# Kernel tuning notes

Measured on AMD Instinct MI355X. Metric: run time of the kernel, lower is better.

Reference implementation:

```python
import jax, jax.numpy as jnp
import numpy as np

NUM_EMBEDDINGS = 8192
EMBEDDING_DIM = 256
COMMITMENT_COST = 0.25
DECAY = 0.99
EPS = 1e-05


def setup_inputs() -> dict:
    key = jax.random.key(0)
    k1, k2, k3 = jax.random.split(key, 3)
    x = jax.random.normal(k1, (16, 256, 32, 32), dtype=jnp.float32)
    emb = jax.random.normal(k2, (NUM_EMBEDDINGS, EMBEDDING_DIM), dtype=jnp.float32) * 0.1
    emb = emb / jnp.linalg.norm(emb, axis=1, keepdims=True)  # F.normalize(dim=1)
    return {
        "x": x,
        "embedding": emb,
        "cluster_size": jnp.ones((NUM_EMBEDDINGS,), dtype=jnp.float32),
        "embed_avg": emb,
    }


def reference(x, embedding, cluster_size, embed_avg):
    K, D = embedding.shape
    n = x.ndim
    # permute channels (dim 1) to last, flatten to [N, D]
    perm_fwd = (0,) + tuple(range(2, n)) + (1,)
    px = jnp.transpose(x, perm_fwd)
    flat = px.reshape(-1, D)  # [N, D]

    # squared L2 distances (monotone in cdist p=2) -> argmin nearest code
    d = (
        jnp.sum(flat * flat, axis=1, keepdims=True)
        - 2.0 * (flat @ embedding.T)
        + jnp.sum(embedding * embedding, axis=1)
    )  # [N, K]
    idx = jnp.argmin(d, axis=1)  # [N]

    # gather-by-index instead of one-hot @ embedding (same math)
    quantized = embedding[idx].reshape(px.shape)
    perm_back = (0, n - 1) + tuple(range(1, n - 1))
    quantized = jnp.transpose(quantized, perm_back)  # back to x layout

    # EMA buffer updates (training path, no_grad in torch)
    counts = jax.ops.segment_sum(
        jnp.ones_like(idx, dtype=flat.dtype), idx, num_segments=K
    )  # == encodings.sum(0)
    new_cluster_size = cluster_size * DECAY + (1.0 - DECAY) * counts
    dw = jax.ops.segment_sum(flat, idx, num_segments=K)  # == encodings.T @ flat
    new_embed_avg = embed_avg * DECAY + (1.0 - DECAY) * dw
    new_embedding = new_embed_avg / jnp.maximum(new_cluster_size, EPS)[:, None]

    # commitment loss (quantized detached)
    loss = COMMITMENT_COST * jnp.mean((x - jax.lax.stop_gradient(quantized)) ** 2)

    # straight-through estimator
    quantized_st = x + jax.lax.stop_gradient(quantized - x)

    avg_probs = counts / flat.shape[0]  # == encodings.mean(0)
    perplexity = jnp.exp(-jnp.sum(avg_probs * jnp.log(avg_probs + 1e-10)))

    return (quantized_st, loss, perplexity, new_embedding, new_cluster_size, new_embed_avg)
```

## Files before the change

### kernel.cpp

```cpp
#include <hip/hip_runtime.h>
#include <stdint.h>

#define K_CODES 8192
#define D 256
#define NROWS 16384
#define NELEM 4194304

#define WS_ENORM   0x00000u
#define WS_KEYS    0x08000u
#define WS_ICOUNTS 0x28000u
#define WS_CURSOR  0x30000u
#define WS_BASE    0x38000u
#define WS_ROWLIST 0x40000u
#define WS_PART    0x50000u
#define WS_XHI     0x60000u
#define WS_XLO     (WS_XHI + 0x800000u)
#define WS_EHI     (WS_XLO + 0x800000u)
#define WS_ELO     (WS_EHI + 0x400000u)

#define O_QST  0
#define O_LOSS 4194304
#define O_PERP 4194305
#define O_EMB  4194306
#define O_CS   6291458
#define O_EAVG 6299650

typedef unsigned short u16;
typedef __attribute__((ext_vector_type(8))) short bf16x8;
typedef __attribute__((ext_vector_type(4))) float f32x4;

__device__ __forceinline__ u16 f2bf(float f) {
    uint32_t u = __float_as_uint(f);
    u += 0x7FFFu + ((u >> 16) & 1u);
    return (u16)(u >> 16);
}
__device__ __forceinline__ float bf2f(u16 h) {
    return __uint_as_float(((uint32_t)h) << 16);
}

__device__ __forceinline__ void glds16(const u16* g, u16* lds_base) {
    __builtin_amdgcn_global_load_lds(
        (const __attribute__((address_space(1))) uint32_t*)g,
        (__attribute__((address_space(3))) uint32_t*)lds_base, 16, 0, 0);
}

__global__ __launch_bounds__(256) void prep_emb_kernel(const float* __restrict__ emb,
                                                       u16* __restrict__ eh,
                                                       u16* __restrict__ el,
                                                       float* __restrict__ enorm) {
    const int k = blockIdx.x, t = threadIdx.x;
    const size_t i = (size_t)k * D + t;
    const float v = emb[i];
    const u16 h = f2bf(v);
    const float r = v - bf2f(h);
    eh[i] = h;
    el[i] = f2bf(r);
    float s = v * v;
#pragma unroll
    for (int off = 32; off; off >>= 1) s += __shfl_down(s, off, 64);
    __shared__ float sm[4];
    if ((t & 63) == 0) sm[t >> 6] = s;
    __syncthreads();
    if (t == 0) enorm[k] = sm[0] + sm[1] + sm[2] + sm[3];
}

__global__ __launch_bounds__(256) void prep_x_kernel(const float* __restrict__ x,
                                                     u16* __restrict__ xhi,
                                                     u16* __restrict__ xlo) {
    __shared__ u16 Lh[64][72];
    __shared__ u16 Ll[64][72];
    const int hw0 = blockIdx.x << 6;
    const int c0 = blockIdx.y << 6;
    const int b = blockIdx.z;
    const int t = threadIdx.x, l = t & 63, w = t >> 6;
#pragma unroll
    for (int i = 0; i < 16; ++i) {
        const int cl = w * 16 + i;
        const float v = x[(((size_t)(b * 256 + c0 + cl)) << 10) + hw0 + l];
        const u16 h = f2bf(v);
        Lh[l][cl] = h;
        Ll[l][cl] = f2bf(v - bf2f(h));
    }
    __syncthreads();
    const int r = t >> 2, cs = t & 3;
    const size_t n = (((size_t)b) << 10) + hw0 + r;
    const size_t o = n * D + c0 + cs * 16;
    *(uint4*)&xhi[o]     = *(const uint4*)&Lh[r][cs * 16];
    *(uint4*)&xhi[o + 8] = *(const uint4*)&Lh[r][cs * 16 + 8];
    *(uint4*)&xlo[o]     = *(const uint4*)&Ll[r][cs * 16];
    *(uint4*)&xlo[o + 8] = *(const uint4*)&Ll[r][cs * 16 + 8];
}

#define BM 128
#define BN 128
#define BK 32
#define SLICES 8
#define CT_PER 8

__global__ __launch_bounds__(256) void dist_kernel(const u16* __restrict__ xhi,
                                                   const u16* __restrict__ xlo,
                                                   const u16* __restrict__ ehi,
                                                   const u16* __restrict__ elo,
                                                   const float* __restrict__ enorm,
                                                   unsigned long long* __restrict__ keys) {
    __shared__ __align__(16) u16 Ah[BM * BK];
    __shared__ __align__(16) u16 Al[BM * BK];
    __shared__ __align__(16) u16 Bh[BN * BK];
    __shared__ __align__(16) u16 Bl[BN * BK];

    const int tid = threadIdx.x;
    const int l = tid & 63, w = tid >> 6;
    const int wr = w >> 1, wc = w & 1;
    const int slice = blockIdx.x;
    const int n0 = blockIdx.y * BM;
    const int md = l & 15, quad = l >> 4;

    const int c0s = w * 64 + l;
    const int row0 = c0s >> 2, s0 = c0s & 3;
    const int g0 = (s0 - ((row0 >> 1) & 3)) & 3;
    const int c1s = 256 + w * 64 + l;
    const int row1 = c1s >> 2, s1 = c1s & 3;
    const int g1 = (s1 - ((row1 >> 1) & 3)) & 3;
    const int ldsb0 = w * 512;
    const int ldsb1 = 2048 + w * 512;
    const size_t aoff0 = (size_t)(n0 + row0) * D + g0 * 8;
    const size_t aoff1 = (size_t)(n0 + row1) * D + g1 * 8;

    const int sA = (quad + ((md >> 1) & 3)) & 3;

    float rbv[4][4];
    int rbi[4][4];
#pragma unroll
    for (int i = 0; i < 4; ++i)
#pragma unroll
        for (int r = 0; r < 4; ++r) { rbv[i][r] = 1e30f; rbi[i][r] = 0; }

    for (int ct = 0; ct < CT_PER; ++ct) {
        const int cbase = (slice * CT_PER + ct) * BN;
        const size_t boff0 = (size_t)(cbase + row0) * D + g0 * 8;
        const size_t boff1 = (size_t)(cbase + row1) * D + g1 * 8;

        f32x4 acc[4][4];
#pragma unroll
        for (int i = 0; i < 4; ++i)
#pragma unroll
            for (int j = 0; j < 4; ++j) acc[i][j] = (f32x4)0.f;

        for (int kt = 0; kt < D / BK; ++kt) {
            const int kc = kt * BK;
            __syncthreads();
            glds16(xhi + aoff0 + kc, &Ah[ldsb0]);
            glds16(xhi + aoff1 + kc, &Ah[ldsb1]);
            glds16(xlo + aoff0 + kc, &Al[ldsb0]);
            glds16(xlo + aoff1 + kc, &Al[ldsb1]);
            glds16(ehi + boff0 + kc, &Bh[ldsb0]);
            glds16(ehi + boff1 + kc, &Bh[ldsb1]);
            glds16(elo + boff0 + kc, &Bl[ldsb0]);
            glds16(elo + boff1 + kc, &Bl[ldsb1]);
            __syncthreads();

            bf16x8 ah[4], al4[4], bh4[4], bl4[4];
#pragma unroll
            for (int i = 0; i < 4; ++i) {
                const int ra = (wr * 64 + i * 16 + md) * BK + sA * 8;
                const int rb = (wc * 64 + i * 16 + md) * BK + sA * 8;
                ah[i]  = *(const bf16x8*)&Ah[ra];
                al4[i] = *(const bf16x8*)&Al[ra];
                bh4[i] = *(const bf16x8*)&Bh[rb];
                bl4[i] = *(const bf16x8*)&Bl[rb];
            }
#pragma unroll
            for (int i = 0; i < 4; ++i)
#pragma unroll
                for (int j = 0; j < 4; ++j) {
                    acc[i][j] = __builtin_amdgcn_mfma_f32_16x16x32_bf16(ah[i],  bh4[j], acc[i][j], 0, 0, 0);
                    acc[i][j] = __builtin_amdgcn_mfma_f32_16x16x32_bf16(ah[i],  bl4[j], acc[i][j], 0, 0, 0);
                    acc[i][j] = __builtin_amdgcn_mfma_f32_16x16x32_bf16(al4[i], bh4[j], acc[i][j], 0, 0, 0);
                }
        }

        float ec[4];
#pragma unroll
        for (int j = 0; j < 4; ++j) ec[j] = enorm[cbase + wc * 64 + j * 16 + md];
#pragma unroll
        for (int i = 0; i < 4; ++i)
#pragma unroll
            for (int r = 0; r < 4; ++r)
#pragma unroll
                for (int j = 0; j < 4; ++j) {
                    const float s = fmaf(-2.f, acc[i][j][r], ec[j]);
                    const int ci = cbase + wc * 64 + j * 16 + md;
                    if (s < rbv[i][r]) { rbv[i][r] = s; rbi[i][r] = ci; }
                }
    }

#pragma unroll
    for (int i = 0; i < 4; ++i)
#pragma unroll
        for (int r = 0; r < 4; ++r) {
            float bv = rbv[i][r];
            int bi = rbi[i][r];
#pragma unroll
            for (int m = 1; m < 16; m <<= 1) {
                const float ov = __shfl_xor(bv, m, 64);
                const int oi = __shfl_xor(bi, m, 64);
                if (ov < bv || (ov == bv && oi < bi)) { bv = ov; bi = oi; }
            }
            if (md == 0) {
                unsigned int u = __float_as_uint(bv);
                u = (u & 0x80000000u) ? ~u : (u | 0x80000000u);
                const unsigned long long key = ((unsigned long long)u << 32) | (unsigned int)bi;
                atomicMin(&keys[n0 + wr * 64 + i * 16 + quad * 4 + r], key);
            }
        }
}

__global__ __launch_bounds__(256) void quant_loss_kernel(const float* __restrict__ x,
                                                         const float* __restrict__ emb,
                                                         const unsigned long long* __restrict__ keys,
                                                         float* __restrict__ out,
                                                         float* __restrict__ partials,
                                                         int* __restrict__ icounts) {
    const int blk = blockIdx.x;
    const int b = blk >> 4;
    const int hw0 = (blk & 15) << 6;
    const int l = threadIdx.x & 63;
    const int cq = threadIdx.x >> 6;
    const int hw = hw0 + l;
    const int n = (b << 10) + hw;
    const int code = (int)(keys[n] & 0xFFFFFFFFull);
    if (threadIdx.x < 64) atomicAdd(&icounts[code], 1);
    const float* erow = emb + (size_t)code * D;
    const float* xb = x + (((size_t)b * 256) << 10) + hw;
    float* ob = out + O_QST + (((size_t)b * 256) << 10) + hw;
    float lsum = 0.f;
#pragma unroll 4
    for (int c = cq; c < D; c += 4) {
        const float xv = xb[(size_t)c << 10];
        const float ev = erow[c];
        ob[(size_t)c << 10] = xv + (ev - xv);
        const float d = xv - ev;
        lsum = fmaf(d, d, lsum);
    }
    __shared__ float sm[4];
    const int lane = threadIdx.x & 63, wv = threadIdx.x >> 6;
#pragma unroll
    for (int off = 32; off; off >>= 1) lsum += __shfl_down(lsum, off, 64);
    if (lane == 0) sm[wv] = lsum;
    __syncthreads();
    if (threadIdx.x == 0) partials[blockIdx.x] = sm[0] + sm[1] + sm[2] + sm[3];
}

__global__ __launch_bounds__(256) void scan_final_kernel(const int* __restrict__ icounts,
                                                         int* __restrict__ basearr,
                                                         const float* __restrict__ partials,
                                                         float* __restrict__ out) {
    const int t = threadIdx.x, lane = t & 63, w = t >> 6;
    int loc = 0;
    float ps = 0.f;
    for (int i = 0; i < 32; ++i) {
        const int c = icounts[t * 32 + i];
        loc += c;
        const float p = (float)c * (1.0f / 16384.0f);
        ps += p * logf(p + 1e-10f);
    }
    int v = loc;
#pragma unroll
    for (int off = 1; off < 64; off <<= 1) {
        const int u = __shfl_up(v, off, 64);
        if (lane >= off) v += u;
    }
    __shared__ int wsum[4];
    __shared__ float fs[8];
    if (lane == 63) wsum[w] = v;
    float lp = partials[t];
#pragma unroll
    for (int off = 32; off; off >>= 1) {
        lp += __shfl_down(lp, off, 64);
        ps += __shfl_down(ps, off, 64);
    }
    if (lane == 0) { fs[w] = lp; fs[4 + w] = ps; }
    __syncthreads();
    int pre = 0;
    for (int i = 0; i < w; ++i) pre += wsum[i];
    int b = pre + v - loc;
    for (int i = 0; i < 32; ++i) {
        basearr[t * 32 + i] = b;
        b += icounts[t * 32 + i];
    }
    if (t == 0) {
        out[O_LOSS] = 0.25f * ((fs[0] + fs[1] + fs[2] + fs[3]) / 4194304.0f);
        out[O_PERP] = expf(-(fs[4] + fs[5] + fs[6] + fs[7]));
    }
}

__global__ __launch_bounds__(256) void slot_kernel(const unsigned long long* __restrict__ keys,
                                                   const int* __restrict__ basearr,
                                                   int* __restrict__ cursor,
                                                   int* __restrict__ rowlist) {
    const int n = blockIdx.x * 256 + threadIdx.x;
    const int code = (int)(keys[n] & 0xFFFFFFFFull);
    const int pos = atomicAdd(&cursor[code], 1);
    rowlist[basearr[code] + pos] = n;
}

__global__ __launch_bounds__(256) void gather_ema_kernel(const u16* __restrict__ xhi,
                                                         const u16* __restrict__ xlo,
                                                         const int* __restrict__ icounts,
                                                         const int* __restrict__ basearr,
                                                         const int* __restrict__ rowlist,
                                                         const float* __restrict__ embed_avg,
                                                         const float* __restrict__ cluster_size,
                                                         float* __restrict__ out) {
    const int k = blockIdx.x, c = threadIdx.x;
    const int cnt = icounts[k], b0 = basearr[k];
    float s = 0.f;
    for (int t = 0; t < cnt; ++t) {
        const int n = rowlist[b0 + t];
        s += bf2f(xhi[(size_t)n * D + c]) + bf2f(xlo[(size_t)n * D + c]);
    }
    const float ncs = cluster_size[k] * 0.99f + 0.01f * (float)cnt;
    const size_t i = (size_t)k * D + c;
    const float na = embed_avg[i] * 0.99f + 0.01f * s;
    out[O_EAVG + i] = na;
    out[O_EMB + i] = na / fmaxf(ncs, 1e-5f);
    if (c == 0) out[O_CS + k] = ncs;
}

extern "C" void kernel_launch(void* const* d_in, const int* in_sizes, int n_in,
                              void* d_out, int out_size, void* d_ws, size_t ws_size,
                              hipStream_t stream) {
    const float* x            = (const float*)d_in[0];
    const float* emb          = (const float*)d_in[1];
    const float* cluster_size = (const float*)d_in[2];
    const float* embed_avg    = (const float*)d_in[3];
    float* out = (float*)d_out;
    char* ws = (char*)d_ws;

    float* enorm = (float*)(ws + WS_ENORM);
    unsigned long long* keys = (unsigned long long*)(ws + WS_KEYS);
    int* icounts = (int*)(ws + WS_ICOUNTS);
    int* cursor = (int*)(ws + WS_CURSOR);
    int* basearr = (int*)(ws + WS_BASE);
    int* rowlist = (int*)(ws + WS_ROWLIST);
    float* partials = (float*)(ws + WS_PART);
    u16* xhi = (u16*)(ws + WS_XHI);
    u16* xlo = (u16*)(ws + WS_XLO);
    u16* ehi = (u16*)(ws + WS_EHI);
    u16* elo = (u16*)(ws + WS_ELO);

    hipMemsetAsync(ws + WS_ICOUNTS, 0, 0x10000, stream);
    hipMemsetAsync(ws + WS_KEYS, 0xFF, NROWS * 8, stream);

    prep_emb_kernel<<<K_CODES, 256, 0, stream>>>(emb, ehi, elo, enorm);
    prep_x_kernel<<<dim3(16, 4, 16), 256, 0, stream>>>(x, xhi, xlo);
    dist_kernel<<<dim3(SLICES, NROWS / BM), 256, 0, stream>>>(xhi, xlo, ehi, elo, enorm, keys);
    quant_loss_kernel<<<256, 256, 0, stream>>>(x, emb, keys, out, partials, icounts);
    scan_final_kernel<<<1, 256, 0, stream>>>(icounts, basearr, partials, out);
    slot_kernel<<<NROWS / 256, 256, 0, stream>>>(keys, basearr, cursor, rowlist);
    gather_ema_kernel<<<K_CODES, 256, 0, stream>>>(xhi, xlo, icounts, basearr, rowlist,
                                                   embed_avg, cluster_size, out);
}
```

Before: 358.1 us.

## Keep full X row tile resident in LDS and double-buffer codebook chunks

The distance kernel now loads the whole 128-row hi/lo X tile (all 256 dims) into 160KB of dynamic LDS once per block, instead of reloading it for every codebook tile. Codebook hi/lo chunks are streamed into a double buffer with one barrier per k-step, so the next chunk's load overlaps the current MFMAs. The grid shrinks to 2 slices of 32 code tiles each, with XOR-swizzled LDS layouts. This cuts redundant global and LDS traffic for X, at the cost of one block per CU and fewer blocks in flight.

Result: faster. 298.7 us (-16.6%).

```diff
diff --git a/kernel.cpp b/kernel.cpp
--- a/kernel.cpp
+++ b/kernel.cpp
@@ -93,20 +93,16 @@
 
 #define BM 128
 #define BN 128
-#define BK 32
-#define SLICES 8
-#define CT_PER 8
-
-__global__ __launch_bounds__(256) void dist_kernel(const u16* __restrict__ xhi,
-                                                   const u16* __restrict__ xlo,
-                                                   const u16* __restrict__ ehi,
-                                                   const u16* __restrict__ elo,
-                                                   const float* __restrict__ enorm,
-                                                   unsigned long long* __restrict__ keys) {
-    __shared__ __align__(16) u16 Ah[BM * BK];
-    __shared__ __align__(16) u16 Al[BM * BK];
-    __shared__ __align__(16) u16 Bh[BN * BK];
-    __shared__ __align__(16) u16 Bl[BN * BK];
+#define SLICES 2
+#define CT_PER 32
+
+__global__ __launch_bounds__(256, 1) void dist_kernel(const u16* __restrict__ xhi,
+                                                      const u16* __restrict__ xlo,
+                                                      const u16* __restrict__ ehi,
+                                                      const u16* __restrict__ elo,
+                                                      const float* __restrict__ enorm,
+                                                      unsigned long long* __restrict__ keys) {
+    extern __shared__ __align__(16) u16 lds[];
 
     const int tid = threadIdx.x;
     const int l = tid & 63, w = tid >> 6;
@@ -115,18 +111,42 @@
     const int n0 = blockIdx.y * BM;
     const int md = l & 15, quad = l >> 4;
 
-    const int c0s = w * 64 + l;
-    const int row0 = c0s >> 2, s0 = c0s & 3;
-    const int g0 = (s0 - ((row0 >> 1) & 3)) & 3;
-    const int c1s = 256 + w * 64 + l;
-    const int row1 = c1s >> 2, s1 = c1s & 3;
-    const int g1 = (s1 - ((row1 >> 1) & 3)) & 3;
-    const int ldsb0 = w * 512;
-    const int ldsb1 = 2048 + w * 512;
-    const size_t aoff0 = (size_t)(n0 + row0) * D + g0 * 8;
-    const size_t aoff1 = (size_t)(n0 + row1) * D + g1 * 8;
-
-    const int sA = (quad + ((md >> 1) & 3)) & 3;
+#pragma unroll
+    for (int wd = 0; wd < 16; ++wd) {
+        const int win = w * 16 + wd;
+        const int rA = 2 * win + (l >> 5);
+        const int g = (l & 31) ^ (rA & 31);
+        const size_t src = (size_t)(n0 + rA) * D + g * 8;
+        glds16(xhi + src, &lds[win * 512]);
+        glds16(xlo + src, &lds[32768 + win * 512]);
+    }
+
+    const int rloc = l >> 3, sB = l & 7, gB = sB ^ rloc;
+    const u16* PB[4];
+#pragma unroll
+    for (int w8 = 0; w8 < 4; ++w8) {
+        const u16* pl = (gB & 4) ? elo : ehi;
+        PB[w8] = pl + (size_t)(slice * 4096 + w * 32 + w8 * 8 + rloc) * D + (gB & 3) * 8;
+    }
+    const int bdst = 65536 + (w * 32) * 64;
+
+#pragma unroll
+    for (int w8 = 0; w8 < 4; ++w8) glds16(PB[w8], &lds[bdst + w8 * 512]);
+
+    int rbase[4], rh[4];
+#pragma unroll
+    for (int i = 0; i < 4; ++i) {
+        const int rA = wr * 64 + i * 16 + md;
+        rbase[i] = rA * 256;
+        rh[i] = rA & 31;
+    }
+    int offBH[4], offBL[4];
+#pragma unroll
+    for (int j = 0; j < 4; ++j) {
+        const int cr = wc * 64 + j * 16 + md;
+        offBH[j] = 65536 + cr * 64 + ((quad) ^ (md & 7)) * 8;
+        offBL[j] = 65536 + cr * 64 + ((quad + 4) ^ (md & 7)) * 8;
+    }
 
     float rbv[4][4];
     int rbi[4][4];
@@ -136,38 +156,37 @@
         for (int r = 0; r < 4; ++r) { rbv[i][r] = 1e30f; rbi[i][r] = 0; }
 
     for (int ct = 0; ct < CT_PER; ++ct) {
-        const int cbase = (slice * CT_PER + ct) * BN;
-        const size_t boff0 = (size_t)(cbase + row0) * D + g0 * 8;
-        const size_t boff1 = (size_t)(cbase + row1) * D + g1 * 8;
-
         f32x4 acc[4][4];
 #pragma unroll
         for (int i = 0; i < 4; ++i)
 #pragma unroll
             for (int j = 0; j < 4; ++j) acc[i][j] = (f32x4)0.f;
 
-        for (int kt = 0; kt < D / BK; ++kt) {
-            const int kc = kt * BK;
+#pragma unroll
+        for (int kt = 0; kt < 8; ++kt) {
             __syncthreads();
-            glds16(xhi + aoff0 + kc, &Ah[ldsb0]);
-            glds16(xhi + aoff1 + kc, &Ah[ldsb1]);
-            glds16(xlo + aoff0 + kc, &Al[ldsb0]);
-            glds16(xlo + aoff1 + kc, &Al[ldsb1]);
-            glds16(ehi + boff0 + kc, &Bh[ldsb0]);
-            glds16(ehi + boff1 + kc, &Bh[ldsb1]);
-            glds16(elo + boff0 + kc, &Bl[ldsb0]);
-            glds16(elo + boff1 + kc, &Bl[ldsb1]);
-            __syncthreads();
-
+            const int m = ct * 8 + kt;
+            if (m < CT_PER * 8 - 1) {
+                const int m1 = m + 1;
+                const int soff = (m1 >> 3) * 32768 + (m1 & 7) * 32;
+                const int db = bdst + ((m1 & 1) << 13);
+#pragma unroll
+                for (int w8 = 0; w8 < 4; ++w8)
+                    glds16(PB[w8] + soff, &lds[db + w8 * 512]);
+            }
+
+            const int bufo = (kt & 1) << 13;
             bf16x8 ah[4], al4[4], bh4[4], bl4[4];
 #pragma unroll
             for (int i = 0; i < 4; ++i) {
-                const int ra = (wr * 64 + i * 16 + md) * BK + sA * 8;
-                const int rb = (wc * 64 + i * 16 + md) * BK + sA * 8;
-                ah[i]  = *(const bf16x8*)&Ah[ra];
-                al4[i] = *(const bf16x8*)&Al[ra];
-                bh4[i] = *(const bf16x8*)&Bh[rb];
-                bl4[i] = *(const bf16x8*)&Bl[rb];
+                const int slot = ((kt << 2) | quad) ^ rh[i];
+                ah[i]  = *(const bf16x8*)&lds[rbase[i] + slot * 8];
+                al4[i] = *(const bf16x8*)&lds[32768 + rbase[i] + slot * 8];
+            }
+#pragma unroll
+            for (int j = 0; j < 4; ++j) {
+                bh4[j] = *(const bf16x8*)&lds[bufo + offBH[j]];
+                bl4[j] = *(const bf16x8*)&lds[bufo + offBL[j]];
             }
 #pragma unroll
             for (int i = 0; i < 4; ++i)
@@ -179,9 +198,10 @@
                 }
         }
 
+        const int gc0 = slice * 4096 + ct * 128;
         float ec[4];
 #pragma unroll
-        for (int j = 0; j < 4; ++j) ec[j] = enorm[cbase + wc * 64 + j * 16 + md];
+        for (int j = 0; j < 4; ++j) ec[j] = enorm[gc0 + wc * 64 + j * 16 + md];
 #pragma unroll
         for (int i = 0; i < 4; ++i)
 #pragma unroll
@@ -189,7 +209,7 @@
 #pragma unroll
                 for (int j = 0; j < 4; ++j) {
                     const float s = fmaf(-2.f, acc[i][j][r], ec[j]);
-                    const int ci = cbase + wc * 64 + j * 16 + md;
+                    const int ci = gc0 + wc * 64 + j * 16 + md;
                     if (s < rbv[i][r]) { rbv[i][r] = s; rbi[i][r] = ci; }
                 }
     }
@@ -349,12 +369,19 @@
     u16* ehi = (u16*)(ws + WS_EHI);
     u16* elo = (u16*)(ws + WS_ELO);
 
+    static int lds_attr_set = 0;
+    if (!lds_attr_set) {
+        hipFuncSetAttribute((const void*)dist_kernel,
+                            hipFuncAttributeMaxDynamicSharedMemorySize, 163840);
+        lds_attr_set = 1;
+    }
+
     hipMemsetAsync(ws + WS_ICOUNTS, 0, 0x10000, stream);
     hipMemsetAsync(ws + WS_KEYS, 0xFF, NROWS * 8, stream);
 
     prep_emb_kernel<<<K_CODES, 256, 0, stream>>>(emb, ehi, elo, enorm);
     prep_x_kernel<<<dim3(16, 4, 16), 256, 0, stream>>>(x, xhi, xlo);
-    dist_kernel<<<dim3(SLICES, NROWS / BM), 256, 0, stream>>>(xhi, xlo, ehi, elo, enorm, keys);
+    dist_kernel<<<dim3(SLICES, NROWS / BM), 256, 163840, stream>>>(xhi, xlo, ehi, elo, enorm, keys);
     quant_loss_kernel<<<256, 256, 0, stream>>>(x, emb, keys, out, partials, icounts);
     scan_final_kernel<<<1, 256, 0, stream>>>(icounts, basearr, partials, out);
     slot_kernel<<<NROWS / 256, 256, 0, stream>>>(keys, basearr, cursor, rowlist);
```

## Pre-pack operands into MFMA fragment layout and restructure distance GEMM with 32x32 MFMA

Applied to the files above, without the earlier changes.

Merges the embedding and x prep kernels plus both memsets into one prep kernel. That kernel writes x and codebook hi/lo bf16 splits directly in a 32x32x16 MFMA fragment-packed layout. The distance kernel now keeps each wave's 32-row A tile in LDS and the lo part in registers. It streams pre-packed B fragments straight from global memory with register double buffering, which removes the per-k-step barriers and LDS staging of B. Gather_ema is updated to index the packed layout; the risks are heavier register pressure, uncoalesced gathers and B reads that are not shared across waves.

After: 412.8 us. +15.3%, slower.

```diff
diff --git a/kernel.cpp b/kernel.cpp
--- a/kernel.cpp
+++ b/kernel.cpp
@@ -13,10 +13,10 @@
 #define WS_BASE    0x38000u
 #define WS_ROWLIST 0x40000u
 #define WS_PART    0x50000u
-#define WS_XHI     0x60000u
-#define WS_XLO     (WS_XHI + 0x800000u)
-#define WS_EHI     (WS_XLO + 0x800000u)
-#define WS_ELO     (WS_EHI + 0x400000u)
+#define WS_APK_HI  0x60000u
+#define WS_APK_LO  (WS_APK_HI + 0x800000u)
+#define WS_BPK_HI  (WS_APK_LO + 0x800000u)
+#define WS_BPK_LO  (WS_BPK_HI + 0x400000u)
 
 #define O_QST  0
 #define O_LOSS 4194304
@@ -27,7 +27,7 @@
 
 typedef unsigned short u16;
 typedef __attribute__((ext_vector_type(8))) short bf16x8;
-typedef __attribute__((ext_vector_type(4))) float f32x4;
+typedef __attribute__((ext_vector_type(16))) float f32x16;
 
 __device__ __forceinline__ u16 f2bf(float f) {
     uint32_t u = __float_as_uint(f);
@@ -44,175 +44,195 @@
         (__attribute__((address_space(3))) uint32_t*)lds_base, 16, 0, 0);
 }
 
-__global__ __launch_bounds__(256) void prep_emb_kernel(const float* __restrict__ emb,
-                                                       u16* __restrict__ eh,
-                                                       u16* __restrict__ el,
-                                                       float* __restrict__ enorm) {
-    const int k = blockIdx.x, t = threadIdx.x;
-    const size_t i = (size_t)k * D + t;
-    const float v = emb[i];
-    const u16 h = f2bf(v);
-    const float r = v - bf2f(h);
-    eh[i] = h;
-    el[i] = f2bf(r);
-    float s = v * v;
-#pragma unroll
-    for (int off = 32; off; off >>= 1) s += __shfl_down(s, off, 64);
-    __shared__ float sm[4];
-    if ((t & 63) == 0) sm[t >> 6] = s;
+
+__global__ __launch_bounds__(256) void prep_kernel(const float* __restrict__ emb,
+                                                   const float* __restrict__ x,
+                                                   u16* __restrict__ apk_hi,
+                                                   u16* __restrict__ apk_lo,
+                                                   u16* __restrict__ bpk_hi,
+                                                   u16* __restrict__ bpk_lo,
+                                                   float* __restrict__ enorm,
+                                                   unsigned long long* __restrict__ keys,
+                                                   int* __restrict__ icounts,
+                                                   int* __restrict__ cursor) {
+    __shared__ u16 Lh[32][264];
+    __shared__ u16 Ll[32][264];
+    const int bid = blockIdx.x, t = threadIdx.x;
+    const int l = t & 63, w = t >> 6;
+
+    if (bid < 512) {
+        const int g = bid;
+        const int b = g >> 5;
+        const int hw0 = (g & 31) << 5;
+        for (int cc = 0; cc < 32; ++cc) {
+            const int c = w * 64 + cc * 2 + (l >> 5);
+            const float v = x[(((size_t)(b * 256 + c)) << 10) + hw0 + (l & 31)];
+            const u16 h = f2bf(v);
+            Lh[l & 31][c] = h;
+            Ll[l & 31][c] = f2bf(v - bf2f(h));
+        }
+        __syncthreads();
+#pragma unroll
+        for (int q = 0; q < 4; ++q) {
+            const int ch = q * 256 + t;
+            const int ks = ch >> 6, lane = ch & 63;
+            const int row = lane & 31;
+            const int kb = ks * 16 + ((lane >> 5) << 3);
+            const size_t o = ((((size_t)g * 16 + ks) * 64) + lane) * 8;
+            *(uint4*)&apk_hi[o] = *(const uint4*)&Lh[row][kb];
+            *(uint4*)&apk_lo[o] = *(const uint4*)&Ll[row][kb];
+        }
+    } else if (bid < 768) {
+        const int g = bid - 512;
+        const int k0 = g << 5;
+        for (int row = 0; row < 32; ++row) {
+            const float v = emb[(size_t)(k0 + row) * D + t];
+            const u16 h = f2bf(v);
+            Lh[row][t] = h;
+            Ll[row][t] = f2bf(v - bf2f(h));
+        }
+        __syncthreads();
+#pragma unroll
+        for (int q = 0; q < 4; ++q) {
+            const int ch = q * 256 + t;
+            const int ks = ch >> 6, lane = ch & 63;
+            const int row = lane & 31;
+            const int kb = ks * 16 + ((lane >> 5) << 3);
+            const size_t o = ((((size_t)g * 16 + ks) * 64) + lane) * 8;
+            *(uint4*)&bpk_hi[o] = *(const uint4*)&Lh[row][kb];
+            *(uint4*)&bpk_lo[o] = *(const uint4*)&Ll[row][kb];
+        }
+        const int row = t >> 3, cq = t & 7;
+        float s = 0.f;
+        for (int c = cq; c < D; c += 8) {
+            const float v = bf2f(Lh[row][c]) + bf2f(Ll[row][c]);
+            s = fmaf(v, v, s);
+        }
+        s += __shfl_xor(s, 1, 64);
+        s += __shfl_xor(s, 2, 64);
+        s += __shfl_xor(s, 4, 64);
+        if (cq == 0) enorm[k0 + row] = s;
+    } else if (bid < 832) {
+        keys[(bid - 768) * 256 + t] = ~0ull;
+    } else {
+        const int m = (bid - 832) * 256 + t;
+        icounts[m] = 0;
+        cursor[m] = 0;
+    }
+}
+
+#define CT_PER 16
+#define NRB 256
+
+__global__ __launch_bounds__(128, 2) void dist_kernel(const u16* __restrict__ apk_hi,
+                                                      const u16* __restrict__ apk_lo,
+                                                      const u16* __restrict__ bpk_hi,
+                                                      const u16* __restrict__ bpk_lo,
+                                                      const float* __restrict__ enorm,
+                                                      unsigned long long* __restrict__ keys) {
+    __shared__ __align__(16) u16 As[16384];
+
+    const int t = threadIdx.x, l = t & 63, w = t >> 6;
+    const int bx = blockIdx.x;
+    const int slice = bx & 3;
+    const int rb = bx >> 2;
+    const int grb = rb * 2 + w;
+
+    const u16* asrc = apk_hi + (((size_t)grb * 16) * 64) * 8 + l * 8;
+    u16* adst = &As[w * 8192];
+#pragma unroll
+    for (int ks = 0; ks < 16; ++ks)
+        glds16(asrc + ks * 512, adst + ks * 512);
+
+    const u16* lsrc = apk_lo + (((size_t)grb * 16) * 64) * 8 + l * 8;
+    bf16x8 falo[16];
+#pragma unroll
+    for (int ks = 0; ks < 16; ++ks)
+        falo[ks] = *(const bf16x8*)(lsrc + ks * 512);
+
     __syncthreads();
-    if (t == 0) enorm[k] = sm[0] + sm[1] + sm[2] + sm[3];
-}
-
-__global__ __launch_bounds__(256) void prep_x_kernel(const float* __restrict__ x,
-                                                     u16* __restrict__ xhi,
-                                                     u16* __restrict__ xlo) {
-    __shared__ u16 Lh[64][72];
-    __shared__ u16 Ll[64][72];
-    const int hw0 = blockIdx.x << 6;
-    const int c0 = blockIdx.y << 6;
-    const int b = blockIdx.z;
-    const int t = threadIdx.x, l = t & 63, w = t >> 6;
-#pragma unroll
-    for (int i = 0; i < 16; ++i) {
-        const int cl = w * 16 + i;
-        const float v = x[(((size_t)(b * 256 + c0 + cl)) << 10) + hw0 + l];
-        const u16 h = f2bf(v);
-        Lh[l][cl] = h;
-        Ll[l][cl] = f2bf(v - bf2f(h));
-    }
-    __syncthreads();
-    const int r = t >> 2, cs = t & 3;
-    const size_t n = (((size_t)b) << 10) + hw0 + r;
-    const size_t o = n * D + c0 + cs * 16;
-    *(uint4*)&xhi[o]     = *(const uint4*)&Lh[r][cs * 16];
-    *(uint4*)&xhi[o + 8] = *(const uint4*)&Lh[r][cs * 16 + 8];
-    *(uint4*)&xlo[o]     = *(const uint4*)&Ll[r][cs * 16];
-    *(uint4*)&xlo[o + 8] = *(const uint4*)&Ll[r][cs * 16 + 8];
-}
-
-#define BM 128
-#define BN 128
-#define BK 32
-#define SLICES 8
-#define CT_PER 8
-
-__global__ __launch_bounds__(256) void dist_kernel(const u16* __restrict__ xhi,
-                                                   const u16* __restrict__ xlo,
-                                                   const u16* __restrict__ ehi,
-                                                   const u16* __restrict__ elo,
-                                                   const float* __restrict__ enorm,
-                                                   unsigned long long* __restrict__ keys) {
-    __shared__ __align__(16) u16 Ah[BM * BK];
-    __shared__ __align__(16) u16 Al[BM * BK];
-    __shared__ __align__(16) u16 Bh[BN * BK];
-    __shared__ __align__(16) u16 Bl[BN * BK];
-
-    const int tid = threadIdx.x;
-    const int l = tid & 63, w = tid >> 6;
-    const int wr = w >> 1, wc = w & 1;
-    const int slice = blockIdx.x;
-    const int n0 = blockIdx.y * BM;
-    const int md = l & 15, quad = l >> 4;
-
-    const int c0s = w * 64 + l;
-    const int row0 = c0s >> 2, s0 = c0s & 3;
-    const int g0 = (s0 - ((row0 >> 1) & 3)) & 3;
-    const int c1s = 256 + w * 64 + l;
-    const int row1 = c1s >> 2, s1 = c1s & 3;
-    const int g1 = (s1 - ((row1 >> 1) & 3)) & 3;
-    const int ldsb0 = w * 512;
-    const int ldsb1 = 2048 + w * 512;
-    const size_t aoff0 = (size_t)(n0 + row0) * D + g0 * 8;
-    const size_t aoff1 = (size_t)(n0 + row1) * D + g1 * 8;
-
-    const int sA = (quad + ((md >> 1) & 3)) & 3;
-
-    float rbv[4][4];
-    int rbi[4][4];
-#pragma unroll
-    for (int i = 0; i < 4; ++i)
-#pragma unroll
-        for (int r = 0; r < 4; ++r) { rbv[i][r] = 1e30f; rbi[i][r] = 0; }
+
+    const u16* bh = bpk_hi + ((size_t)slice * 64 * 16) * 512 + l * 8;
+    const u16* bl = bpk_lo + ((size_t)slice * 64 * 16) * 512 + l * 8;
+
+    float rbv[16];
+    int rbi[16];
+#pragma unroll
+    for (int r = 0; r < 16; ++r) { rbv[r] = 1e30f; rbi[r] = 0; }
+
+    f32x16 acc[4];
+#pragma unroll
+    for (int j = 0; j < 4; ++j) acc[j] = (f32x16)0.f;
+
+    bf16x8 fb[2][8], ahf[2];
+#pragma unroll
+    for (int j = 0; j < 4; ++j) {
+        const int off = (j * 16) * 512;
+        fb[0][j * 2]     = *(const bf16x8*)(bh + off);
+        fb[0][j * 2 + 1] = *(const bf16x8*)(bl + off);
+    }
+    ahf[0] = *(const bf16x8*)&As[w * 8192 + l * 8];
 
     for (int ct = 0; ct < CT_PER; ++ct) {
-        const int cbase = (slice * CT_PER + ct) * BN;
-        const size_t boff0 = (size_t)(cbase + row0) * D + g0 * 8;
-        const size_t boff1 = (size_t)(cbase + row1) * D + g1 * 8;
-
-        f32x4 acc[4][4];
-#pragma unroll
-        for (int i = 0; i < 4; ++i)
-#pragma unroll
-            for (int j = 0; j < 4; ++j) acc[i][j] = (f32x4)0.f;
-
-        for (int kt = 0; kt < D / BK; ++kt) {
-            const int kc = kt * BK;
-            __syncthreads();
-            glds16(xhi + aoff0 + kc, &Ah[ldsb0]);
-            glds16(xhi + aoff1 + kc, &Ah[ldsb1]);
-            glds16(xlo + aoff0 + kc, &Al[ldsb0]);
-            glds16(xlo + aoff1 + kc, &Al[ldsb1]);
-            glds16(ehi + boff0 + kc, &Bh[ldsb0]);
-            glds16(ehi + boff1 + kc, &Bh[ldsb1]);
-            glds16(elo + boff0 + kc, &Bl[ldsb0]);
-            glds16(elo + boff1 + kc, &Bl[ldsb1]);
-            __syncthreads();
-
-            bf16x8 ah[4], al4[4], bh4[4], bl4[4];
-#pragma unroll
-            for (int i = 0; i < 4; ++i) {
-                const int ra = (wr * 64 + i * 16 + md) * BK + sA * 8;
-                const int rb = (wc * 64 + i * 16 + md) * BK + sA * 8;
-                ah[i]  = *(const bf16x8*)&Ah[ra];
-                al4[i] = *(const bf16x8*)&Al[ra];
-                bh4[i] = *(const bf16x8*)&Bh[rb];
-                bl4[i] = *(const bf16x8*)&Bl[rb];
+        __builtin_amdgcn_s_barrier();
+        const int cbase = slice * 2048 + ct * 128;
+        float ecr[4];
+#pragma unroll
+        for (int j = 0; j < 4; ++j) ecr[j] = enorm[cbase + j * 32 + (l & 31)];
+
+#pragma unroll
+        for (int ks = 0; ks < 16; ++ks) {
+            const int p = ks & 1, nx = p ^ 1;
+            if (ct * 16 + ks < CT_PER * 16 - 1) {
+                const int nct = (ks == 15) ? ct + 1 : ct;
+                const int nks = (ks + 1) & 15;
+#pragma unroll
+                for (int j = 0; j < 4; ++j) {
+                    const int off = ((nct * 4 + j) * 16 + nks) * 512;
+                    fb[nx][j * 2]     = *(const bf16x8*)(bh + off);
+                    fb[nx][j * 2 + 1] = *(const bf16x8*)(bl + off);
+                }
             }
-#pragma unroll
-            for (int i = 0; i < 4; ++i)
-#pragma unroll
-                for (int j = 0; j < 4; ++j) {
-                    acc[i][j] = __builtin_amdgcn_mfma_f32_16x16x32_bf16(ah[i],  bh4[j], acc[i][j], 0, 0, 0);
-                    acc[i][j] = __builtin_amdgcn_mfma_f32_16x16x32_bf16(ah[i],  bl4[j], acc[i][j], 0, 0, 0);
-                    acc[i][j] = __builtin_amdgcn_mfma_f32_16x16x32_bf16(al4[i], bh4[j], acc[i][j], 0, 0, 0);
-                }
-        }
-
-        float ec[4];
-#pragma unroll
-        for (int j = 0; j < 4; ++j) ec[j] = enorm[cbase + wc * 64 + j * 16 + md];
-#pragma unroll
-        for (int i = 0; i < 4; ++i)
-#pragma unroll
-            for (int r = 0; r < 4; ++r)
-#pragma unroll
-                for (int j = 0; j < 4; ++j) {
-                    const float s = fmaf(-2.f, acc[i][j][r], ec[j]);
-                    const int ci = cbase + wc * 64 + j * 16 + md;
-                    if (s < rbv[i][r]) { rbv[i][r] = s; rbi[i][r] = ci; }
-                }
-    }
-
-#pragma unroll
-    for (int i = 0; i < 4; ++i)
-#pragma unroll
-        for (int r = 0; r < 4; ++r) {
-            float bv = rbv[i][r];
-            int bi = rbi[i][r];
-#pragma unroll
-            for (int m = 1; m < 16; m <<= 1) {
-                const float ov = __shfl_xor(bv, m, 64);
-                const int oi = __shfl_xor(bi, m, 64);
-                if (ov < bv || (ov == bv && oi < bi)) { bv = ov; bi = oi; }
+            ahf[nx] = *(const bf16x8*)&As[w * 8192 + ((ks + 1) & 15) * 512 + l * 8];
+#pragma unroll
+            for (int j = 0; j < 4; ++j) {
+                acc[j] = __builtin_amdgcn_mfma_f32_32x32x16_bf16(ahf[p],   fb[p][j * 2],     acc[j], 0, 0, 0);
+                acc[j] = __builtin_amdgcn_mfma_f32_32x32x16_bf16(ahf[p],   fb[p][j * 2 + 1], acc[j], 0, 0, 0);
+                acc[j] = __builtin_amdgcn_mfma_f32_32x32x16_bf16(falo[ks], fb[p][j * 2],     acc[j], 0, 0, 0);
             }
-            if (md == 0) {
-                unsigned int u = __float_as_uint(bv);
-                u = (u & 0x80000000u) ? ~u : (u | 0x80000000u);
-                const unsigned long long key = ((unsigned long long)u << 32) | (unsigned int)bi;
-                atomicMin(&keys[n0 + wr * 64 + i * 16 + quad * 4 + r], key);
+        }
+
+#pragma unroll
+        for (int j = 0; j < 4; ++j) {
+            const int ci = cbase + j * 32 + (l & 31);
+#pragma unroll
+            for (int r = 0; r < 16; ++r) {
+                const float s = fmaf(-2.f, acc[j][r], ecr[j]);
+                if (s < rbv[r]) { rbv[r] = s; rbi[r] = ci; }
+                acc[j][r] = 0.f;
             }
         }
+    }
+
+#pragma unroll
+    for (int r = 0; r < 16; ++r) {
+        float bv = rbv[r];
+        int bi = rbi[r];
+#pragma unroll
+        for (int m = 1; m < 32; m <<= 1) {
+            const float ov = __shfl_xor(bv, m, 64);
+            const int oi = __shfl_xor(bi, m, 64);
+            if (ov < bv || (ov == bv && oi < bi)) { bv = ov; bi = oi; }
+        }
+        if ((l & 31) == 0) {
+            const int row = (r & 3) + 8 * (r >> 2) + 4 * (l >> 5);
+            const int n = rb * 64 + w * 32 + row;
+            unsigned int u = __float_as_uint(bv);
+            u = (u & 0x80000000u) ? ~u : (u | 0x80000000u);
+            const unsigned long long key = ((unsigned long long)u << 32) | (unsigned int)bi;
+            atomicMin(&keys[n], key);
+        }
+    }
 }
 
 __global__ __launch_bounds__(256) void quant_loss_kernel(const float* __restrict__ x,
@@ -304,8 +324,8 @@
     rowlist[basearr[code] + pos] = n;
 }
 
-__global__ __launch_bounds__(256) void gather_ema_kernel(const u16* __restrict__ xhi,
-                                                         const u16* __restrict__ xlo,
+__global__ __launch_bounds__(256) void gather_ema_kernel(const u16* __restrict__ apk_hi,
+                                                         const u16* __restrict__ apk_lo,
                                                          const int* __restrict__ icounts,
                                                          const int* __restrict__ basearr,
                                                          const int* __restrict__ rowlist,
@@ -314,10 +334,12 @@
                                                          float* __restrict__ out) {
     const int k = blockIdx.x, c = threadIdx.x;
     const int cnt = icounts[k], b0 = basearr[k];
+    const int ks = c >> 4, lhalf = (c >> 3) & 1, e = c & 7;
     float s = 0.f;
     for (int t = 0; t < cnt; ++t) {
         const int n = rowlist[b0 + t];
-        s += bf2f(xhi[(size_t)n * D + c]) + bf2f(xlo[(size_t)n * D + c]);
+        const size_t o = ((((size_t)(n >> 5) * 16 + ks) * 64) + (lhalf << 5) + (n & 31)) * 8 + e;
+        s += bf2f(apk_hi[o]) + bf2f(apk_lo[o]);
     }
     const float ncs = cluster_size[k] * 0.99f + 0.01f * (float)cnt;
     const size_t i = (size_t)k * D + c;
@@ -344,20 +366,17 @@
     int* basearr = (int*)(ws + WS_BASE);
     int* rowlist = (int*)(ws + WS_ROWLIST);
     float* partials = (float*)(ws + WS_PART);
-    u16* xhi = (u16*)(ws + WS_XHI);
-    u16* xlo = (u16*)(ws + WS_XLO);
-    u16* ehi = (u16*)(ws + WS_EHI);
-    u16* elo = (u16*)(ws + WS_ELO);
-
-    hipMemsetAsync(ws + WS_ICOUNTS, 0, 0x10000, stream);
-    hipMemsetAsync(ws + WS_KEYS, 0xFF, NROWS * 8, stream);
-
-    prep_emb_kernel<<<K_CODES, 256, 0, stream>>>(emb, ehi, elo, enorm);
-    prep_x_kernel<<<dim3(16, 4, 16), 256, 0, stream>>>(x, xhi, xlo);
-    dist_kernel<<<dim3(SLICES, NROWS / BM), 256, 0, stream>>>(xhi, xlo, ehi, elo, enorm, keys);
+    u16* apk_hi = (u16*)(ws + WS_APK_HI);
+    u16* apk_lo = (u16*)(ws + WS_APK_LO);
+    u16* bpk_hi = (u16*)(ws + WS_BPK_HI);
+    u16* bpk_lo = (u16*)(ws + WS_BPK_LO);
+
+    prep_kernel<<<864, 256, 0, stream>>>(emb, x, apk_hi, apk_lo, bpk_hi, bpk_lo,
+                                         enorm, keys, icounts, cursor);
+    dist_kernel<<<1024, 128, 0, stream>>>(apk_hi, apk_lo, bpk_hi, bpk_lo, enorm, keys);
     quant_loss_kernel<<<256, 256, 0, stream>>>(x, emb, keys, out, partials, icounts);
     scan_final_kernel<<<1, 256, 0, stream>>>(icounts, basearr, partials, out);
     slot_kernel<<<NROWS / 256, 256, 0, stream>>>(keys, basearr, cursor, rowlist);
-    gather_ema_kernel<<<K_CODES, 256, 0, stream>>>(xhi, xlo, icounts, basearr, rowlist,
+    gather_ema_kernel<<<K_CODES, 256, 0, stream>>>(apk_hi, apk_lo, icounts, basearr, rowlist,
                                                    embed_avg, cluster_size, out);
 }
```
